# Performance work log

Measured on AMD Instinct MI355X. Metric: run time of the kernel, lower is better.

The kernel has to match this reference:

```python
import jax, jax.numpy as jnp
import numpy as np

SEQ_LEN, BATCH, D_IN, H = 2048, 1, 2048, 2048


def setup_inputs() -> dict:
    key = jax.random.key(0)
    ks = jax.random.split(key, 10)
    s_in = 1.0 / np.sqrt(D_IN)
    s_h = 1.0 / np.sqrt(H)
    return {
        "x": jax.random.normal(ks[0], (SEQ_LEN, BATCH, D_IN), jnp.float32),
        "h": jax.random.normal(ks[1], (BATCH, H), jnp.float32),
        "Wfx": jax.random.uniform(ks[2], (H, D_IN), jnp.float32, -s_in, s_in),
        "bfx": jax.random.uniform(ks[3], (H,), jnp.float32, -s_in, s_in),
        "Wfh": jax.random.uniform(ks[4], (H, H), jnp.float32, -s_h, s_h),
        "bfh": jax.random.uniform(ks[5], (H,), jnp.float32, -s_h, s_h),
        "Whf": jax.random.uniform(ks[6], (H, H), jnp.float32, -s_h, s_h),
        "bhf": jax.random.uniform(ks[7], (H,), jnp.float32, -s_h, s_h),
        "Whx": jax.random.uniform(ks[8], (H, D_IN), jnp.float32, -s_in, s_in),
        "bhx": jax.random.uniform(ks[9], (H,), jnp.float32, -s_in, s_in),
    }


def reference(x, h, Wfx, bfx, Wfh, bfh, Whf, bhf, Whx, bhx):
    # Precompute input projections for all timesteps (same math, batched GEMM).
    xf = jnp.einsum("sbd,hd->sbh", x, Wfx) + bfx  # [S, B, H]
    xh = jnp.einsum("sbd,hd->sbh", x, Whx) + bhx  # [S, B, H]

    def step(h, inp):
        xf_t, xh_t = inp
        f = jax.nn.sigmoid(xf_t + h @ Wfh.T + bfh)
        h_hat = jnp.tanh((f * h) @ Whf.T + bhf + xh_t)
        h_new = (1.0 - f) * h + f * h_hat
        return h_new, h_new[-1]  # y[i] = h[-1]

    h_final, y = jax.lax.scan(step, h, (xf, xh))
    return y[:, None, :], h_final  # y: [S, 1, H]
```

## Files before the change

kernel.cpp:

```cpp
#include <hip/hip_runtime.h>
#include <math.h>


#define S_LEN 2048
#define HDIM  2048
#define DDIM  2048
#define NWG   256
#define ROWS  8
#define SCAN_BLK 256
#define QELEM (HDIM / SCAN_BLK)

typedef unsigned long long ull;

__global__ __launch_bounds__(256) void xproj_gemm(
    const float* __restrict__ x,
    const float* __restrict__ Wfx, const float* __restrict__ bfx, const float* __restrict__ bfh,
    const float* __restrict__ Whx, const float* __restrict__ bhx, const float* __restrict__ bhf,
    float* __restrict__ XF, float* __restrict__ XH)
{
    const float* W  = blockIdx.z ? Whx : Wfx;
    const float* b1 = blockIdx.z ? bhx : bfx;
    const float* b2 = blockIdx.z ? bhf : bfh;
    float* out      = blockIdx.z ? XH  : XF;

    __shared__ float As[16][64];
    __shared__ float Bs[16][64];

    const int tid = threadIdx.x;
    const int s0 = blockIdx.y * 64;
    const int h0 = blockIdx.x * 64;
    const int lr = tid >> 2;
    const int lk = (tid & 3) << 2;
    const int ty = tid >> 4;
    const int tx = tid & 15;

    float acc[4][4];
#pragma unroll
    for (int i = 0; i < 4; ++i)
#pragma unroll
        for (int j = 0; j < 4; ++j) acc[i][j] = 0.f;

    for (int k0 = 0; k0 < DDIM; k0 += 16) {
        float4 av = *(const float4*)&x[(size_t)(s0 + lr) * DDIM + k0 + lk];
        float4 bv = *(const float4*)&W[(size_t)(h0 + lr) * DDIM + k0 + lk];
        As[lk + 0][lr] = av.x; As[lk + 1][lr] = av.y; As[lk + 2][lr] = av.z; As[lk + 3][lr] = av.w;
        Bs[lk + 0][lr] = bv.x; Bs[lk + 1][lr] = bv.y; Bs[lk + 2][lr] = bv.z; Bs[lk + 3][lr] = bv.w;
        __syncthreads();
#pragma unroll
        for (int kk = 0; kk < 16; ++kk) {
            float4 a4 = *(const float4*)&As[kk][ty << 2];
            float4 b4 = *(const float4*)&Bs[kk][tx << 2];
            float ar[4] = {a4.x, a4.y, a4.z, a4.w};
            float br[4] = {b4.x, b4.y, b4.z, b4.w};
#pragma unroll
            for (int i = 0; i < 4; ++i)
#pragma unroll
                for (int j = 0; j < 4; ++j)
                    acc[i][j] = fmaf(ar[i], br[j], acc[i][j]);
        }
        __syncthreads();
    }

    float4 bv1 = *(const float4*)&b1[h0 + (tx << 2)];
    float4 bv2 = *(const float4*)&b2[h0 + (tx << 2)];
    float bb[4] = {bv1.x + bv2.x, bv1.y + bv2.y, bv1.z + bv2.z, bv1.w + bv2.w};
#pragma unroll
    for (int i = 0; i < 4; ++i) {
        int s = s0 + (ty << 2) + i;
        float4 o;
        o.x = acc[i][0] + bb[0];
        o.y = acc[i][1] + bb[1];
        o.z = acc[i][2] + bb[2];
        o.w = acc[i][3] + bb[3];
        *(float4*)&out[(size_t)s * HDIM + h0 + (tx << 2)] = o;
    }
}

__device__ __forceinline__ void publish_tagged(ull* buf, int idx, unsigned epoch, float v)
{
    ull w = ((ull)epoch << 32) | (ull)__float_as_uint(v);
    __hip_atomic_store(&buf[idx], w, __ATOMIC_RELAXED, __HIP_MEMORY_SCOPE_AGENT);
}

__device__ __forceinline__ void gather_tagged(const ull* buf, unsigned target,
                                              float* lds, int tid, int& bail)
{
    if (!bail) {
        int guard = 0;
        for (;;) {
            ull w[QELEM];
#pragma unroll
            for (int q = 0; q < QELEM; ++q)
                w[q] = __hip_atomic_load(&buf[tid + q * SCAN_BLK],
                                         __ATOMIC_RELAXED, __HIP_MEMORY_SCOPE_AGENT);
            bool ok = true;
#pragma unroll
            for (int q = 0; q < QELEM; ++q)
                ok = ok && ((unsigned)(w[q] >> 32) == target);
            if (ok) {
#pragma unroll
                for (int q = 0; q < QELEM; ++q)
                    lds[tid + q * SCAN_BLK] = __uint_as_float((unsigned)w[q]);
                break;
            }
            if (++guard > (1 << 18)) { bail = 1; break; }
        }
    }
    __syncthreads();
}

__global__ __launch_bounds__(SCAN_BLK) void mgu_scan(
    const float* __restrict__ h0,
    const float* __restrict__ Wfh,
    const float* __restrict__ Whf,
    const float* __restrict__ XF,
    const float* __restrict__ XH,
    float* __restrict__ y,
    float* __restrict__ hfin,
    ull* h_buf, ull* g_buf)
{
    extern __shared__ float smem[];
    float* wf    = smem;
    float* wh    = wf + ROWS * HDIM;
    float* h_lds = wh + ROWS * HDIM;
    float* g_lds = h_lds + HDIM;

    const int wg   = blockIdx.x;
    const int tid  = threadIdx.x;
    const int lane = tid & 63;
    const int wv   = tid >> 6;
    const int base = wg * ROWS;

    for (int i = tid; i < ROWS * HDIM / 4; i += SCAN_BLK) {
        ((float4*)wf)[i] = ((const float4*)(Wfh + (size_t)base * HDIM))[i];
        ((float4*)wh)[i] = ((const float4*)(Whf + (size_t)base * HDIM))[i];
    }
    if (tid < ROWS)
        publish_tagged(h_buf, base + tid, 1u, h0[base + tid]);
    __syncthreads();

    const int r0 = wv * 2, r1 = wv * 2 + 1;
    int bail = 0;

    for (int t = 0; t < S_LEN; ++t) {
        float xf0 = XF[(size_t)t * HDIM + base + r0];
        float xf1 = XF[(size_t)t * HDIM + base + r1];
        float xh0 = XH[(size_t)t * HDIM + base + r0];
        float xh1 = XH[(size_t)t * HDIM + base + r1];

        gather_tagged(h_buf, (unsigned)(t + 1), h_lds, tid, bail);

        float4 a0 = {0, 0, 0, 0}, a1 = {0, 0, 0, 0};
#pragma unroll
        for (int it = 0; it < HDIM / 256; ++it) {
            int j = it * 256 + (lane << 2);
            float4 hv = *(const float4*)&h_lds[j];
            float4 w0 = *(const float4*)&wf[r0 * HDIM + j];
            float4 w1 = *(const float4*)&wf[r1 * HDIM + j];
            a0.x = fmaf(w0.x, hv.x, a0.x); a0.y = fmaf(w0.y, hv.y, a0.y);
            a0.z = fmaf(w0.z, hv.z, a0.z); a0.w = fmaf(w0.w, hv.w, a0.w);
            a1.x = fmaf(w1.x, hv.x, a1.x); a1.y = fmaf(w1.y, hv.y, a1.y);
            a1.z = fmaf(w1.z, hv.z, a1.z); a1.w = fmaf(w1.w, hv.w, a1.w);
        }
        float s0 = (a0.x + a0.y) + (a0.z + a0.w);
        float s1 = (a1.x + a1.y) + (a1.z + a1.w);
#pragma unroll
        for (int m = 32; m >= 1; m >>= 1) {
            s0 += __shfl_xor(s0, m);
            s1 += __shfl_xor(s1, m);
        }
        float f0 = 0.f, f1 = 0.f, ho0 = 0.f, ho1 = 0.f;
        if (lane == 0) {
            f0 = 1.f / (1.f + expf(-(s0 + xf0)));
            f1 = 1.f / (1.f + expf(-(s1 + xf1)));
            ho0 = h_lds[base + r0];
            ho1 = h_lds[base + r1];
            publish_tagged(g_buf, base + r0, (unsigned)(t + 1), f0 * ho0);
            publish_tagged(g_buf, base + r1, (unsigned)(t + 1), f1 * ho1);
        }

        gather_tagged(g_buf, (unsigned)(t + 1), g_lds, tid, bail);

        a0 = make_float4(0, 0, 0, 0); a1 = make_float4(0, 0, 0, 0);
#pragma unroll
        for (int it = 0; it < HDIM / 256; ++it) {
            int j = it * 256 + (lane << 2);
            float4 gv = *(const float4*)&g_lds[j];
            float4 w0 = *(const float4*)&wh[r0 * HDIM + j];
            float4 w1 = *(const float4*)&wh[r1 * HDIM + j];
            a0.x = fmaf(w0.x, gv.x, a0.x); a0.y = fmaf(w0.y, gv.y, a0.y);
            a0.z = fmaf(w0.z, gv.z, a0.z); a0.w = fmaf(w0.w, gv.w, a0.w);
            a1.x = fmaf(w1.x, gv.x, a1.x); a1.y = fmaf(w1.y, gv.y, a1.y);
            a1.z = fmaf(w1.z, gv.z, a1.z); a1.w = fmaf(w1.w, gv.w, a1.w);
        }
        s0 = (a0.x + a0.y) + (a0.z + a0.w);
        s1 = (a1.x + a1.y) + (a1.z + a1.w);
#pragma unroll
        for (int m = 32; m >= 1; m >>= 1) {
            s0 += __shfl_xor(s0, m);
            s1 += __shfl_xor(s1, m);
        }
        if (lane == 0) {
            float hh0 = tanhf(s0 + xh0);
            float hh1 = tanhf(s1 + xh1);
            float hn0 = ho0 + f0 * (hh0 - ho0);
            float hn1 = ho1 + f1 * (hh1 - ho1);
            y[(size_t)t * HDIM + base + r0] = hn0;
            y[(size_t)t * HDIM + base + r1] = hn1;
            publish_tagged(h_buf, base + r0, (unsigned)(t + 2), hn0);
            publish_tagged(h_buf, base + r1, (unsigned)(t + 2), hn1);
            if (t == S_LEN - 1) {
                hfin[base + r0] = hn0;
                hfin[base + r1] = hn1;
            }
        }
    }
}

extern "C" void kernel_launch(void* const* d_in, const int* in_sizes, int n_in,
                              void* d_out, int out_size, void* d_ws, size_t ws_size,
                              hipStream_t stream)
{
    const float* x   = (const float*)d_in[0];
    const float* h0  = (const float*)d_in[1];
    const float* Wfx = (const float*)d_in[2];
    const float* bfx = (const float*)d_in[3];
    const float* Wfh = (const float*)d_in[4];
    const float* bfh = (const float*)d_in[5];
    const float* Whf = (const float*)d_in[6];
    const float* bhf = (const float*)d_in[7];
    const float* Whx = (const float*)d_in[8];
    const float* bhx = (const float*)d_in[9];

    float* y    = (float*)d_out;
    float* hfin = y + (size_t)S_LEN * HDIM;

    float* XF  = (float*)d_ws;
    float* XH  = XF + (size_t)S_LEN * HDIM;
    ull* h_buf = (ull*)(XH + (size_t)S_LEN * HDIM);
    ull* g_buf = h_buf + HDIM;

    dim3 gg(HDIM / 64, S_LEN / 64, 2);
    xproj_gemm<<<gg, 256, 0, stream>>>(x, Wfx, bfx, bfh, Whx, bhx, bhf, XF, XH);

    const int smem_bytes = (2 * ROWS * HDIM + 2 * HDIM) * (int)sizeof(float);
    hipFuncSetAttribute((const void*)mgu_scan,
                        hipFuncAttributeMaxDynamicSharedMemorySize, smem_bytes);

    void* args[] = {(void*)&h0, (void*)&Wfh, (void*)&Whf, (void*)&XF, (void*)&XH,
                    (void*)&y, (void*)&hfin, (void*)&h_buf, (void*)&g_buf};
    hipError_t err = hipLaunchCooperativeKernel((void*)mgu_scan, dim3(NWG), dim3(SCAN_BLK),
                                                args, (unsigned)smem_bytes, stream);
    if (err != hipSuccess) {
        mgu_scan<<<dim3(NWG), dim3(SCAN_BLK), smem_bytes, stream>>>(
            h0, Wfh, Whf, XF, XH, y, hfin, h_buf, g_buf);
    }
}
```

Measured before the change: 19.85 ms.

## Replace tagged-payload polling with per-wave flag array wait before payload gather

Adds per-wavefront epoch flags (1024 per phase) that producers write after publishing their tagged values. One wave polls the compact flag array until every flag matches the epoch, then all threads load the payload once, with a per-element retry kept as a fallback. The aim is to stop all 256 threads from repeatedly polling 2048 64-bit words across the device, which cuts coherent polling traffic. In exchange there is an extra global store per wave and an extra __syncthreads per phase, and the payloads and flags are written with relaxed ordering only, so visibility of the payload after a flag is seen is not guaranteed.

```diff
diff --git a/kernel.cpp b/kernel.cpp
--- a/kernel.cpp
+++ b/kernel.cpp
@@ -9,6 +9,8 @@
 #define ROWS  8
 #define SCAN_BLK 256
 #define QELEM (HDIM / SCAN_BLK)
+#define NFLAG (NWG * 4)
+#define FPL   (NFLAG / 64)
 
 typedef unsigned long long ull;
 
@@ -82,31 +84,53 @@
     __hip_atomic_store(&buf[idx], w, __ATOMIC_RELAXED, __HIP_MEMORY_SCOPE_AGENT);
 }
 
-__device__ __forceinline__ void gather_tagged(const ull* buf, unsigned target,
-                                              float* lds, int tid, int& bail)
-{
-    if (!bail) {
-        int guard = 0;
-        for (;;) {
-            ull w[QELEM];
-#pragma unroll
-            for (int q = 0; q < QELEM; ++q)
-                w[q] = __hip_atomic_load(&buf[tid + q * SCAN_BLK],
-                                         __ATOMIC_RELAXED, __HIP_MEMORY_SCOPE_AGENT);
-            bool ok = true;
-#pragma unroll
-            for (int q = 0; q < QELEM; ++q)
-                ok = ok && ((unsigned)(w[q] >> 32) == target);
-            if (ok) {
-#pragma unroll
-                for (int q = 0; q < QELEM; ++q)
-                    lds[tid + q * SCAN_BLK] = __uint_as_float((unsigned)w[q]);
-                break;
+__device__ __forceinline__ void flag_wait(const unsigned* flags, unsigned target,
+                                          int lane, int& bail)
+{
+    if (bail) return;
+    int guard = 0;
+    for (;;) {
+        unsigned v[FPL];
+#pragma unroll
+        for (int q = 0; q < FPL; ++q)
+            v[q] = __hip_atomic_load(&flags[lane + q * 64],
+                                     __ATOMIC_RELAXED, __HIP_MEMORY_SCOPE_AGENT);
+        int ok = 1;
+#pragma unroll
+        for (int q = 0; q < FPL; ++q)
+            ok &= (v[q] == target) ? 1 : 0;
+        if (__all(ok)) break;
+        if (++guard > (1 << 18)) { bail = 1; break; }
+    }
+}
+
+__device__ __forceinline__ void gather_payload(const ull* buf, unsigned target,
+                                               float* lds, int tid, int& bail)
+{
+    ull w[QELEM];
+#pragma unroll
+    for (int q = 0; q < QELEM; ++q)
+        w[q] = __hip_atomic_load(&buf[tid + q * SCAN_BLK],
+                                 __ATOMIC_RELAXED, __HIP_MEMORY_SCOPE_AGENT);
+    unsigned miss = 0;
+#pragma unroll
+    for (int q = 0; q < QELEM; ++q)
+        miss |= ((unsigned)(w[q] >> 32) != target) ? (1u << q) : 0u;
+    int guard = 0;
+    while (miss && !bail) {
+#pragma unroll
+        for (int q = 0; q < QELEM; ++q) {
+            if (miss & (1u << q)) {
+                ull v = __hip_atomic_load(&buf[tid + q * SCAN_BLK],
+                                          __ATOMIC_RELAXED, __HIP_MEMORY_SCOPE_AGENT);
+                if ((unsigned)(v >> 32) == target) { w[q] = v; miss &= ~(1u << q); }
             }
-            if (++guard > (1 << 18)) { bail = 1; break; }
-        }
-    }
-    __syncthreads();
+        }
+        if (++guard > (1 << 18)) bail = 1;
+    }
+#pragma unroll
+    for (int q = 0; q < QELEM; ++q)
+        lds[tid + q * SCAN_BLK] = __uint_as_float((unsigned)w[q]);
 }
 
 __global__ __launch_bounds__(SCAN_BLK) void mgu_scan(
@@ -117,7 +141,8 @@
     const float* __restrict__ XH,
     float* __restrict__ y,
     float* __restrict__ hfin,
-    ull* h_buf, ull* g_buf)
+    ull* h_buf, ull* g_buf,
+    unsigned* hflag, unsigned* gflag)
 {
     extern __shared__ float smem[];
     float* wf    = smem;
@@ -138,6 +163,9 @@
     if (tid < ROWS)
         publish_tagged(h_buf, base + tid, 1u, h0[base + tid]);
     __syncthreads();
+    if (tid < 4)
+        __hip_atomic_store(&hflag[wg * 4 + tid], 1u,
+                           __ATOMIC_RELAXED, __HIP_MEMORY_SCOPE_AGENT);
 
     const int r0 = wv * 2, r1 = wv * 2 + 1;
     int bail = 0;
@@ -148,7 +176,10 @@
         float xh0 = XH[(size_t)t * HDIM + base + r0];
         float xh1 = XH[(size_t)t * HDIM + base + r1];
 
-        gather_tagged(h_buf, (unsigned)(t + 1), h_lds, tid, bail);
+        if (wv == 0) flag_wait(hflag, (unsigned)(t + 1), lane, bail);
+        __syncthreads();
+        gather_payload(h_buf, (unsigned)(t + 1), h_lds, tid, bail);
+        __syncthreads();
 
         float4 a0 = {0, 0, 0, 0}, a1 = {0, 0, 0, 0};
 #pragma unroll
@@ -177,9 +208,14 @@
             ho1 = h_lds[base + r1];
             publish_tagged(g_buf, base + r0, (unsigned)(t + 1), f0 * ho0);
             publish_tagged(g_buf, base + r1, (unsigned)(t + 1), f1 * ho1);
-        }
-
-        gather_tagged(g_buf, (unsigned)(t + 1), g_lds, tid, bail);
+            __hip_atomic_store(&gflag[wg * 4 + wv], (unsigned)(t + 1),
+                               __ATOMIC_RELAXED, __HIP_MEMORY_SCOPE_AGENT);
+        }
+
+        if (wv == 0) flag_wait(gflag, (unsigned)(t + 1), lane, bail);
+        __syncthreads();
+        gather_payload(g_buf, (unsigned)(t + 1), g_lds, tid, bail);
+        __syncthreads();
 
         a0 = make_float4(0, 0, 0, 0); a1 = make_float4(0, 0, 0, 0);
 #pragma unroll
@@ -209,6 +245,8 @@
             y[(size_t)t * HDIM + base + r1] = hn1;
             publish_tagged(h_buf, base + r0, (unsigned)(t + 2), hn0);
             publish_tagged(h_buf, base + r1, (unsigned)(t + 2), hn1);
+            __hip_atomic_store(&hflag[wg * 4 + wv], (unsigned)(t + 2),
+                               __ATOMIC_RELAXED, __HIP_MEMORY_SCOPE_AGENT);
             if (t == S_LEN - 1) {
                 hfin[base + r0] = hn0;
                 hfin[base + r1] = hn1;
@@ -235,10 +273,12 @@
     float* y    = (float*)d_out;
     float* hfin = y + (size_t)S_LEN * HDIM;
 
-    float* XF  = (float*)d_ws;
-    float* XH  = XF + (size_t)S_LEN * HDIM;
-    ull* h_buf = (ull*)(XH + (size_t)S_LEN * HDIM);
-    ull* g_buf = h_buf + HDIM;
+    float* XF      = (float*)d_ws;
+    float* XH      = XF + (size_t)S_LEN * HDIM;
+    ull* h_buf     = (ull*)(XH + (size_t)S_LEN * HDIM);
+    ull* g_buf     = h_buf + HDIM;
+    unsigned* hflag = (unsigned*)(g_buf + HDIM);
+    unsigned* gflag = hflag + NFLAG;
 
     dim3 gg(HDIM / 64, S_LEN / 64, 2);
     xproj_gemm<<<gg, 256, 0, stream>>>(x, Wfx, bfx, bfh, Whx, bhx, bhf, XF, XH);
@@ -248,11 +288,12 @@
                         hipFuncAttributeMaxDynamicSharedMemorySize, smem_bytes);
 
     void* args[] = {(void*)&h0, (void*)&Wfh, (void*)&Whf, (void*)&XF, (void*)&XH,
-                    (void*)&y, (void*)&hfin, (void*)&h_buf, (void*)&g_buf};
+                    (void*)&y, (void*)&hfin, (void*)&h_buf, (void*)&g_buf,
+                    (void*)&hflag, (void*)&gflag};
     hipError_t err = hipLaunchCooperativeKernel((void*)mgu_scan, dim3(NWG), dim3(SCAN_BLK),
                                                 args, (unsigned)smem_bytes, stream);
     if (err != hipSuccess) {
         mgu_scan<<<dim3(NWG), dim3(SCAN_BLK), smem_bytes, stream>>>(
-            h0, Wfh, Whf, XF, XH, y, hfin, h_buf, g_buf);
-    }
-}
+            h0, Wfh, Whf, XF, XH, y, hfin, h_buf, g_buf, hflag, gflag);
+    }
+}
```

Result: slower. 22.92 ms (+15.5%).

## Replace per-element tagged polling with per-workgroup flags plus bulk payload read

Applied to the files above, without the earlier changes.

Replaces the scheme where every thread polls 64-bit epoch-tagged values across the whole hidden vector with separate float payload buffers and one flag per workgroup. One wavefront polls 256 flags (with s_sleep backoff), then all threads read the payload in bulk into LDS. Payload and flag writes use relaxed atomic exchanges, relying on RMW ordering instead of explicit release/acquire fences. This cuts polling traffic but adds extra __syncthreads per step and risks stale reads if payload visibility is not guaranteed before the flag.

```diff
diff --git a/kernel.cpp b/kernel.cpp
--- a/kernel.cpp
+++ b/kernel.cpp
@@ -9,8 +9,6 @@
 #define ROWS  8
 #define SCAN_BLK 256
 #define QELEM (HDIM / SCAN_BLK)
-
-typedef unsigned long long ull;
 
 __global__ __launch_bounds__(256) void xproj_gemm(
     const float* __restrict__ x,
@@ -76,37 +74,40 @@
     }
 }
 
-__device__ __forceinline__ void publish_tagged(ull* buf, int idx, unsigned epoch, float v)
-{
-    ull w = ((ull)epoch << 32) | (ull)__float_as_uint(v);
-    __hip_atomic_store(&buf[idx], w, __ATOMIC_RELAXED, __HIP_MEMORY_SCOPE_AGENT);
-}
-
-__device__ __forceinline__ void gather_tagged(const ull* buf, unsigned target,
-                                              float* lds, int tid, int& bail)
-{
-    if (!bail) {
-        int guard = 0;
-        for (;;) {
-            ull w[QELEM];
-#pragma unroll
-            for (int q = 0; q < QELEM; ++q)
-                w[q] = __hip_atomic_load(&buf[tid + q * SCAN_BLK],
-                                         __ATOMIC_RELAXED, __HIP_MEMORY_SCOPE_AGENT);
-            bool ok = true;
-#pragma unroll
-            for (int q = 0; q < QELEM; ++q)
-                ok = ok && ((unsigned)(w[q] >> 32) == target);
-            if (ok) {
-#pragma unroll
-                for (int q = 0; q < QELEM; ++q)
-                    lds[tid + q * SCAN_BLK] = __uint_as_float((unsigned)w[q]);
-                break;
-            }
-            if (++guard > (1 << 18)) { bail = 1; break; }
-        }
-    }
-    __syncthreads();
+__device__ __forceinline__ void publish_rmw(float* buf, int idx, float v)
+{
+    float old = __hip_atomic_exchange(&buf[idx], v,
+                                      __ATOMIC_RELAXED, __HIP_MEMORY_SCOPE_AGENT);
+    asm volatile("" :: "v"(old));
+}
+
+__device__ __forceinline__ void poll_flags(const unsigned* flags, unsigned target,
+                                           int lane, int& bail)
+{
+    if (bail) return;
+    int guard = 0;
+    for (;;) {
+        unsigned v0 = __hip_atomic_load(&flags[lane],       __ATOMIC_RELAXED, __HIP_MEMORY_SCOPE_AGENT);
+        unsigned v1 = __hip_atomic_load(&flags[lane + 64],  __ATOMIC_RELAXED, __HIP_MEMORY_SCOPE_AGENT);
+        unsigned v2 = __hip_atomic_load(&flags[lane + 128], __ATOMIC_RELAXED, __HIP_MEMORY_SCOPE_AGENT);
+        unsigned v3 = __hip_atomic_load(&flags[lane + 192], __ATOMIC_RELAXED, __HIP_MEMORY_SCOPE_AGENT);
+        int ok = (v0 == target) & (v1 == target) & (v2 == target) & (v3 == target);
+        if (__all(ok)) break;
+        if (++guard > (1 << 18)) { bail = 1; break; }
+        if (guard > 4) __builtin_amdgcn_s_sleep(2);
+    }
+}
+
+__device__ __forceinline__ void bulk_read(const float* pay, float* lds, int tid)
+{
+    float v[QELEM];
+#pragma unroll
+    for (int q = 0; q < QELEM; ++q)
+        v[q] = __hip_atomic_load(&pay[tid + q * SCAN_BLK],
+                                 __ATOMIC_RELAXED, __HIP_MEMORY_SCOPE_AGENT);
+#pragma unroll
+    for (int q = 0; q < QELEM; ++q)
+        lds[tid + q * SCAN_BLK] = v[q];
 }
 
 __global__ __launch_bounds__(SCAN_BLK) void mgu_scan(
@@ -117,7 +118,8 @@
     const float* __restrict__ XH,
     float* __restrict__ y,
     float* __restrict__ hfin,
-    ull* h_buf, ull* g_buf)
+    float* h_pay, float* g_pay,
+    unsigned* hflag, unsigned* gflag)
 {
     extern __shared__ float smem[];
     float* wf    = smem;
@@ -136,8 +138,11 @@
         ((float4*)wh)[i] = ((const float4*)(Whf + (size_t)base * HDIM))[i];
     }
     if (tid < ROWS)
-        publish_tagged(h_buf, base + tid, 1u, h0[base + tid]);
+        publish_rmw(h_pay, base + tid, h0[base + tid]);
     __syncthreads();
+    if (tid == 0)
+        (void)__hip_atomic_exchange(&hflag[wg], 1u,
+                                    __ATOMIC_RELAXED, __HIP_MEMORY_SCOPE_AGENT);
 
     const int r0 = wv * 2, r1 = wv * 2 + 1;
     int bail = 0;
@@ -148,7 +153,10 @@
         float xh0 = XH[(size_t)t * HDIM + base + r0];
         float xh1 = XH[(size_t)t * HDIM + base + r1];
 
-        gather_tagged(h_buf, (unsigned)(t + 1), h_lds, tid, bail);
+        if (wv == 0) poll_flags(hflag, (unsigned)(t + 1), lane, bail);
+        __syncthreads();
+        bulk_read(h_pay, h_lds, tid);
+        __syncthreads();
 
         float4 a0 = {0, 0, 0, 0}, a1 = {0, 0, 0, 0};
 #pragma unroll
@@ -175,11 +183,18 @@
             f1 = 1.f / (1.f + expf(-(s1 + xf1)));
             ho0 = h_lds[base + r0];
             ho1 = h_lds[base + r1];
-            publish_tagged(g_buf, base + r0, (unsigned)(t + 1), f0 * ho0);
-            publish_tagged(g_buf, base + r1, (unsigned)(t + 1), f1 * ho1);
-        }
-
-        gather_tagged(g_buf, (unsigned)(t + 1), g_lds, tid, bail);
+            publish_rmw(g_pay, base + r0, f0 * ho0);
+            publish_rmw(g_pay, base + r1, f1 * ho1);
+        }
+        __syncthreads();
+        if (tid == 0)
+            (void)__hip_atomic_exchange(&gflag[wg], (unsigned)(t + 1),
+                                        __ATOMIC_RELAXED, __HIP_MEMORY_SCOPE_AGENT);
+
+        if (wv == 0) poll_flags(gflag, (unsigned)(t + 1), lane, bail);
+        __syncthreads();
+        bulk_read(g_pay, g_lds, tid);
+        __syncthreads();
 
         a0 = make_float4(0, 0, 0, 0); a1 = make_float4(0, 0, 0, 0);
 #pragma unroll
@@ -207,13 +222,17 @@
             float hn1 = ho1 + f1 * (hh1 - ho1);
             y[(size_t)t * HDIM + base + r0] = hn0;
             y[(size_t)t * HDIM + base + r1] = hn1;
-            publish_tagged(h_buf, base + r0, (unsigned)(t + 2), hn0);
-            publish_tagged(h_buf, base + r1, (unsigned)(t + 2), hn1);
+            publish_rmw(h_pay, base + r0, hn0);
+            publish_rmw(h_pay, base + r1, hn1);
             if (t == S_LEN - 1) {
                 hfin[base + r0] = hn0;
                 hfin[base + r1] = hn1;
             }
         }
+        __syncthreads();
+        if (tid == 0)
+            (void)__hip_atomic_exchange(&hflag[wg], (unsigned)(t + 2),
+                                        __ATOMIC_RELAXED, __HIP_MEMORY_SCOPE_AGENT);
     }
 }
 
@@ -235,10 +254,12 @@
     float* y    = (float*)d_out;
     float* hfin = y + (size_t)S_LEN * HDIM;
 
-    float* XF  = (float*)d_ws;
-    float* XH  = XF + (size_t)S_LEN * HDIM;
-    ull* h_buf = (ull*)(XH + (size_t)S_LEN * HDIM);
-    ull* g_buf = h_buf + HDIM;
+    float* XF       = (float*)d_ws;
+    float* XH       = XF + (size_t)S_LEN * HDIM;
+    float* h_pay    = XH + (size_t)S_LEN * HDIM;
+    float* g_pay    = h_pay + HDIM;
+    unsigned* hflag = (unsigned*)(g_pay + HDIM);
+    unsigned* gflag = hflag + NWG;
 
     dim3 gg(HDIM / 64, S_LEN / 64, 2);
     xproj_gemm<<<gg, 256, 0, stream>>>(x, Wfx, bfx, bfh, Whx, bhx, bhf, XF, XH);
@@ -248,11 +269,12 @@
                         hipFuncAttributeMaxDynamicSharedMemorySize, smem_bytes);
 
     void* args[] = {(void*)&h0, (void*)&Wfh, (void*)&Whf, (void*)&XF, (void*)&XH,
-                    (void*)&y, (void*)&hfin, (void*)&h_buf, (void*)&g_buf};
+                    (void*)&y, (void*)&hfin, (void*)&h_pay, (void*)&g_pay,
+                    (void*)&hflag, (void*)&gflag};
     hipError_t err = hipLaunchCooperativeKernel((void*)mgu_scan, dim3(NWG), dim3(SCAN_BLK),
                                                 args, (unsigned)smem_bytes, stream);
     if (err != hipSuccess) {
         mgu_scan<<<dim3(NWG), dim3(SCAN_BLK), smem_bytes, stream>>>(
-            h0, Wfh, Whf, XF, XH, y, hfin, h_buf, g_buf);
-    }
-}
+            h0, Wfh, Whf, XF, XH, y, hfin, h_pay, g_pay, hflag, gflag);
+    }
+}
```

Result: slower. 24.10 ms (+21.4%).

## Split each recurrent row across two waves with 1024-thread scan blocks

Applied to the files above, without the earlier changes.

The scan workgroup grows from 4 to 16 waves. Each of the 8 rows per workgroup is now split across two waves that each handle half of the 2048-long dot product, and the halves are combined through an LDS partial buffer after a barrier. The tagged-buffer polling now latches each element as it arrives instead of retrying the whole set. It also inserts s_sleep between polls to cut contention on the global flags. The intent is to shorten the per-step dot-product latency, at the cost of an extra block barrier per phase and more polling waves.

```diff
diff --git a/kernel.cpp b/kernel.cpp
--- a/kernel.cpp
+++ b/kernel.cpp
@@ -7,7 +7,7 @@
 #define DDIM  2048
 #define NWG   256
 #define ROWS  8
-#define SCAN_BLK 256
+#define SCAN_BLK 1024
 #define QELEM (HDIM / SCAN_BLK)
 
 typedef unsigned long long ull;
@@ -87,23 +87,15 @@
 {
     if (!bail) {
         int guard = 0;
+        unsigned done = 0;
         for (;;) {
-            ull w[QELEM];
-#pragma unroll
-            for (int q = 0; q < QELEM; ++q)
-                w[q] = __hip_atomic_load(&buf[tid + q * SCAN_BLK],
-                                         __ATOMIC_RELAXED, __HIP_MEMORY_SCOPE_AGENT);
-            bool ok = true;
-#pragma unroll
-            for (int q = 0; q < QELEM; ++q)
-                ok = ok && ((unsigned)(w[q] >> 32) == target);
-            if (ok) {
-#pragma unroll
-                for (int q = 0; q < QELEM; ++q)
-                    lds[tid + q * SCAN_BLK] = __uint_as_float((unsigned)w[q]);
-                break;
-            }
+            ull w0 = __hip_atomic_load(&buf[tid],            __ATOMIC_RELAXED, __HIP_MEMORY_SCOPE_AGENT);
+            ull w1 = __hip_atomic_load(&buf[tid + SCAN_BLK], __ATOMIC_RELAXED, __HIP_MEMORY_SCOPE_AGENT);
+            if ((unsigned)(w0 >> 32) == target) { lds[tid]            = __uint_as_float((unsigned)w0); done |= 1u; }
+            if ((unsigned)(w1 >> 32) == target) { lds[tid + SCAN_BLK] = __uint_as_float((unsigned)w1); done |= 2u; }
+            if (done == 3u) break;
             if (++guard > (1 << 18)) { bail = 1; break; }
+            __builtin_amdgcn_s_sleep(1);
         }
     }
     __syncthreads();
@@ -124,12 +116,16 @@
     float* wh    = wf + ROWS * HDIM;
     float* h_lds = wh + ROWS * HDIM;
     float* g_lds = h_lds + HDIM;
+    float* part  = g_lds + HDIM;
 
     const int wg   = blockIdx.x;
     const int tid  = threadIdx.x;
     const int lane = tid & 63;
     const int wv   = tid >> 6;
+    const int row  = wv >> 1;
+    const int half = wv & 1;
     const int base = wg * ROWS;
+    const bool owner = (half == 0) && (lane == 0);
 
     for (int i = tid; i < ROWS * HDIM / 4; i += SCAN_BLK) {
         ((float4*)wf)[i] = ((const float4*)(Wfh + (size_t)base * HDIM))[i];
@@ -139,80 +135,64 @@
         publish_tagged(h_buf, base + tid, 1u, h0[base + tid]);
     __syncthreads();
 
-    const int r0 = wv * 2, r1 = wv * 2 + 1;
     int bail = 0;
+    float f_r = 0.f, ho_r = 0.f;
 
     for (int t = 0; t < S_LEN; ++t) {
-        float xf0 = XF[(size_t)t * HDIM + base + r0];
-        float xf1 = XF[(size_t)t * HDIM + base + r1];
-        float xh0 = XH[(size_t)t * HDIM + base + r0];
-        float xh1 = XH[(size_t)t * HDIM + base + r1];
+        float xf_r = 0.f, xh_r = 0.f;
+        if (owner) {
+            xf_r = XF[(size_t)t * HDIM + base + row];
+            xh_r = XH[(size_t)t * HDIM + base + row];
+        }
 
         gather_tagged(h_buf, (unsigned)(t + 1), h_lds, tid, bail);
 
-        float4 a0 = {0, 0, 0, 0}, a1 = {0, 0, 0, 0};
-#pragma unroll
-        for (int it = 0; it < HDIM / 256; ++it) {
-            int j = it * 256 + (lane << 2);
+        float4 a = {0, 0, 0, 0};
+#pragma unroll
+        for (int it = 0; it < 4; ++it) {
+            int j = half * 1024 + it * 256 + (lane << 2);
             float4 hv = *(const float4*)&h_lds[j];
-            float4 w0 = *(const float4*)&wf[r0 * HDIM + j];
-            float4 w1 = *(const float4*)&wf[r1 * HDIM + j];
-            a0.x = fmaf(w0.x, hv.x, a0.x); a0.y = fmaf(w0.y, hv.y, a0.y);
-            a0.z = fmaf(w0.z, hv.z, a0.z); a0.w = fmaf(w0.w, hv.w, a0.w);
-            a1.x = fmaf(w1.x, hv.x, a1.x); a1.y = fmaf(w1.y, hv.y, a1.y);
-            a1.z = fmaf(w1.z, hv.z, a1.z); a1.w = fmaf(w1.w, hv.w, a1.w);
-        }
-        float s0 = (a0.x + a0.y) + (a0.z + a0.w);
-        float s1 = (a1.x + a1.y) + (a1.z + a1.w);
-#pragma unroll
-        for (int m = 32; m >= 1; m >>= 1) {
-            s0 += __shfl_xor(s0, m);
-            s1 += __shfl_xor(s1, m);
-        }
-        float f0 = 0.f, f1 = 0.f, ho0 = 0.f, ho1 = 0.f;
-        if (lane == 0) {
-            f0 = 1.f / (1.f + expf(-(s0 + xf0)));
-            f1 = 1.f / (1.f + expf(-(s1 + xf1)));
-            ho0 = h_lds[base + r0];
-            ho1 = h_lds[base + r1];
-            publish_tagged(g_buf, base + r0, (unsigned)(t + 1), f0 * ho0);
-            publish_tagged(g_buf, base + r1, (unsigned)(t + 1), f1 * ho1);
+            float4 w0 = *(const float4*)&wf[row * HDIM + j];
+            a.x = fmaf(w0.x, hv.x, a.x); a.y = fmaf(w0.y, hv.y, a.y);
+            a.z = fmaf(w0.z, hv.z, a.z); a.w = fmaf(w0.w, hv.w, a.w);
+        }
+        float s = (a.x + a.y) + (a.z + a.w);
+#pragma unroll
+        for (int m = 32; m >= 1; m >>= 1) s += __shfl_xor(s, m);
+        if (lane == 0) part[wv] = s;
+        __syncthreads();
+
+        if (owner) {
+            float tot = part[wv] + part[wv + 1];
+            f_r  = 1.f / (1.f + expf(-(tot + xf_r)));
+            ho_r = h_lds[base + row];
+            publish_tagged(g_buf, base + row, (unsigned)(t + 1), f_r * ho_r);
         }
 
         gather_tagged(g_buf, (unsigned)(t + 1), g_lds, tid, bail);
 
-        a0 = make_float4(0, 0, 0, 0); a1 = make_float4(0, 0, 0, 0);
-#pragma unroll
-        for (int it = 0; it < HDIM / 256; ++it) {
-            int j = it * 256 + (lane << 2);
+        a = make_float4(0, 0, 0, 0);
+#pragma unroll
+        for (int it = 0; it < 4; ++it) {
+            int j = half * 1024 + it * 256 + (lane << 2);
             float4 gv = *(const float4*)&g_lds[j];
-            float4 w0 = *(const float4*)&wh[r0 * HDIM + j];
-            float4 w1 = *(const float4*)&wh[r1 * HDIM + j];
-            a0.x = fmaf(w0.x, gv.x, a0.x); a0.y = fmaf(w0.y, gv.y, a0.y);
-            a0.z = fmaf(w0.z, gv.z, a0.z); a0.w = fmaf(w0.w, gv.w, a0.w);
-            a1.x = fmaf(w1.x, gv.x, a1.x); a1.y = fmaf(w1.y, gv.y, a1.y);
-            a1.z = fmaf(w1.z, gv.z, a1.z); a1.w = fmaf(w1.w, gv.w, a1.w);
-        }
-        s0 = (a0.x + a0.y) + (a0.z + a0.w);
-        s1 = (a1.x + a1.y) + (a1.z + a1.w);
-#pragma unroll
-        for (int m = 32; m >= 1; m >>= 1) {
-            s0 += __shfl_xor(s0, m);
-            s1 += __shfl_xor(s1, m);
-        }
-        if (lane == 0) {
-            float hh0 = tanhf(s0 + xh0);
-            float hh1 = tanhf(s1 + xh1);
-            float hn0 = ho0 + f0 * (hh0 - ho0);
-            float hn1 = ho1 + f1 * (hh1 - ho1);
-            y[(size_t)t * HDIM + base + r0] = hn0;
-            y[(size_t)t * HDIM + base + r1] = hn1;
-            publish_tagged(h_buf, base + r0, (unsigned)(t + 2), hn0);
-            publish_tagged(h_buf, base + r1, (unsigned)(t + 2), hn1);
-            if (t == S_LEN - 1) {
-                hfin[base + r0] = hn0;
-                hfin[base + r1] = hn1;
-            }
+            float4 w0 = *(const float4*)&wh[row * HDIM + j];
+            a.x = fmaf(w0.x, gv.x, a.x); a.y = fmaf(w0.y, gv.y, a.y);
+            a.z = fmaf(w0.z, gv.z, a.z); a.w = fmaf(w0.w, gv.w, a.w);
+        }
+        s = (a.x + a.y) + (a.z + a.w);
+#pragma unroll
+        for (int m = 32; m >= 1; m >>= 1) s += __shfl_xor(s, m);
+        if (lane == 0) part[wv] = s;
+        __syncthreads();
+
+        if (owner) {
+            float tot = part[wv] + part[wv + 1];
+            float hh  = tanhf(tot + xh_r);
+            float hn  = ho_r + f_r * (hh - ho_r);
+            y[(size_t)t * HDIM + base + row] = hn;
+            publish_tagged(h_buf, base + row, (unsigned)(t + 2), hn);
+            if (t == S_LEN - 1) hfin[base + row] = hn;
         }
     }
 }
@@ -243,7 +223,7 @@
     dim3 gg(HDIM / 64, S_LEN / 64, 2);
     xproj_gemm<<<gg, 256, 0, stream>>>(x, Wfx, bfx, bfh, Whx, bhx, bhf, XF, XH);
 
-    const int smem_bytes = (2 * ROWS * HDIM + 2 * HDIM) * (int)sizeof(float);
+    const int smem_bytes = (2 * ROWS * HDIM + 2 * HDIM + 16) * (int)sizeof(float);
     hipFuncSetAttribute((const void*)mgu_scan,
                         hipFuncAttributeMaxDynamicSharedMemorySize, smem_bytes);
 
```

New measurement: 21.53 ms. 1.08x slower.
